# Optimization experiments

Hardware: AMD Instinct MI355X
Metric: run time of the kernel (lower is better)

The kernel has to match this reference:

```python
import jax, jax.numpy as jnp
import numpy as np

N_NODES = 50000
N_EDGES = 1_600_000
N_HEADS = 8
IN_DIM = 512
OUT_DIM = 64
LRELU_ALPHA = 0.2


def setup_inputs() -> dict:
    key = jax.random.key(0)
    k1, k2, k3, k4, k5 = jax.random.split(key, 5)
    x = jax.random.normal(k1, (N_NODES, IN_DIM), dtype=jnp.float32)
    # glorot-ish scale for weights
    W = jax.random.normal(k2, (N_HEADS, IN_DIM, OUT_DIM), dtype=jnp.float32) * (1.0 / np.sqrt(IN_DIM))
    att_w = jax.random.normal(k3, (N_HEADS, 2 * OUT_DIM), dtype=jnp.float32) * (1.0 / np.sqrt(2 * OUT_DIM))
    src = jax.random.randint(k4, (N_EDGES,), 0, N_NODES, dtype=jnp.int64 if jax.config.read('jax_enable_x64') else jnp.int32).astype(jnp.int32)
    dst = jax.random.randint(k5, (N_EDGES,), 0, N_NODES, dtype=jnp.int32)
    return {"x": x, "W": W, "att_w": att_w, "src": src, "dst": dst}


def reference(x, W, att_w, src, dst):
    # GAT forward (eval mode: dropout=0, bias off, heads concatenated).
    # attention score: leaky_relu([f_src || f_dst] @ a) == leaky_relu(a1.f_src + a2.f_dst)
    outs = []
    for h in range(N_HEADS):
        feat = x @ W[h]                               # [N, F]
        a1 = att_w[h, :OUT_DIM]                       # [F]
        a2 = att_w[h, OUT_DIM:]                       # [F]
        alpha_s = feat @ a1                           # [N]
        alpha_d = feat @ a2                           # [N]
        logit = jax.nn.leaky_relu(alpha_s[src] + alpha_d[dst], LRELU_ALPHA)  # [E]
        # sparse row-wise softmax over segments keyed by src (row index)
        m = jax.ops.segment_max(logit, src, num_segments=N_NODES)
        e = jnp.exp(logit - m[src])
        denom = jax.ops.segment_sum(e, src, num_segments=N_NODES)
        att = e / denom[src]                          # [E]
        # sparse-dense aggregation: out[row] = sum_edges att * feat[col]
        agg = jax.ops.segment_sum(att[:, None] * feat[dst], src, num_segments=N_NODES)  # [N, F]
        outs.append(jax.nn.relu(agg))                 # act per head (average_heads=False)
    return jnp.concatenate(outs, axis=1)              # [N, H*F]
```

## Files before the change

kernel.cpp:

```cpp
#include <hip/hip_runtime.h>
#include <math.h>

#define N_NODES   50000
#define N_EDGES   1600000
#define N_HEADS   8
#define IN_DIM    512
#define OUT_DIM   64
#define FEAT_DIM  512
#define LRELU_A   0.2f
#define M_TILES   391
#define M_PAD     (M_TILES*128)
#define SCAN_BLK  49

typedef __attribute__((ext_vector_type(8))) short bf16x8;
typedef __attribute__((ext_vector_type(4))) float f32x4;

__device__ inline unsigned short f2bf(float f) {
    unsigned int u = __float_as_uint(f);
    u = (u + 0x7FFFu + ((u >> 16) & 1u)) >> 16;
    return (unsigned short)u;
}
__device__ inline float bf2f(short s) {
    return __uint_as_float(((unsigned int)(unsigned short)s) << 16);
}

__global__ __launch_bounds__(256) void convert_x(const float* __restrict__ x,
                                                 unsigned short* __restrict__ xh) {
    int i = blockIdx.x * blockDim.x + threadIdx.x;
    if (i >= N_NODES * IN_DIM / 4) return;
    float4 v = ((const float4*)x)[i];
    ushort4 o;
    o.x = f2bf(v.x); o.y = f2bf(v.y); o.z = f2bf(v.z); o.w = f2bf(v.w);
    ((ushort4*)xh)[i] = o;
}

__global__ __launch_bounds__(256) void prep_b(const float* __restrict__ W,
                                              unsigned short* __restrict__ Bt) {
    int t = blockIdx.x * blockDim.x + threadIdx.x;
    if (t >= FEAT_DIM * IN_DIM) return;
    int n = t >> 9, k = t & 511;
    int h = n >> 6, o = n & 63;
    Bt[t] = f2bf(W[(size_t)h * IN_DIM * OUT_DIM + (size_t)k * OUT_DIM + o]);
}

__global__ __launch_bounds__(256) void gemm_mfma(const unsigned short* __restrict__ xh,
                                                 const unsigned short* __restrict__ Bt,
                                                 unsigned short* __restrict__ feat_h) {
    __shared__ __align__(16) unsigned short As[128 * 32];
    __shared__ __align__(16) unsigned short Bs[128 * 32];
    const int t    = threadIdx.x;
    const int wid  = t >> 6;
    const int lane = t & 63;
    const int m0   = blockIdx.x * 128;
    const int n0   = blockIdx.y * 128;
    const int wm   = (wid >> 1) * 64;
    const int wn   = (wid & 1) * 64;
    const int mr   = lane & 15;
    const int q    = lane >> 4;

    f32x4 acc[4][4];
    #pragma unroll
    for (int i = 0; i < 4; ++i)
        #pragma unroll
        for (int j = 0; j < 4; ++j) acc[i][j] = 0.0f;

    const char* xb = (const char*)xh;
    const char* bb = (const char*)Bt;
    const int o1 = t * 16;         const int row1 = o1 >> 6, kb1 = o1 & 63;
    const int o2 = t * 16 + 4096;  const int row2 = o2 >> 6, kb2 = o2 & 63;
    char* lA1 = ((char*)As) + wid * 1024;
    char* lA2 = ((char*)As) + 4096 + wid * 1024;
    char* lB1 = ((char*)Bs) + wid * 1024;
    char* lB2 = ((char*)Bs) + 4096 + wid * 1024;

    for (int k0 = 0; k0 < IN_DIM; k0 += 32) {
        const int kbyte = k0 * 2;
        __builtin_amdgcn_global_load_lds(
            (const __attribute__((address_space(1))) unsigned int*)(xb + (size_t)(m0 + row1) * (IN_DIM * 2) + kbyte + kb1),
            (__attribute__((address_space(3))) unsigned int*)lA1, 16, 0, 0);
        __builtin_amdgcn_global_load_lds(
            (const __attribute__((address_space(1))) unsigned int*)(xb + (size_t)(m0 + row2) * (IN_DIM * 2) + kbyte + kb2),
            (__attribute__((address_space(3))) unsigned int*)lA2, 16, 0, 0);
        __builtin_amdgcn_global_load_lds(
            (const __attribute__((address_space(1))) unsigned int*)(bb + (size_t)(n0 + row1) * (IN_DIM * 2) + kbyte + kb1),
            (__attribute__((address_space(3))) unsigned int*)lB1, 16, 0, 0);
        __builtin_amdgcn_global_load_lds(
            (const __attribute__((address_space(1))) unsigned int*)(bb + (size_t)(n0 + row2) * (IN_DIM * 2) + kbyte + kb2),
            (__attribute__((address_space(3))) unsigned int*)lB2, 16, 0, 0);
        __syncthreads();

        bf16x8 a[4], b[4];
        #pragma unroll
        for (int i = 0; i < 4; ++i)
            a[i] = *(const bf16x8*)&As[(wm + i * 16 + mr) * 32 + q * 8];
        #pragma unroll
        for (int j = 0; j < 4; ++j)
            b[j] = *(const bf16x8*)&Bs[(wn + j * 16 + mr) * 32 + q * 8];
        #pragma unroll
        for (int i = 0; i < 4; ++i)
            #pragma unroll
            for (int j = 0; j < 4; ++j)
                acc[i][j] = __builtin_amdgcn_mfma_f32_16x16x32_bf16(a[i], b[j], acc[i][j], 0, 0, 0);
        __syncthreads();
    }

    #pragma unroll
    for (int i = 0; i < 4; ++i) {
        #pragma unroll
        for (int j = 0; j < 4; ++j) {
            int col = n0 + wn + j * 16 + mr;
            #pragma unroll
            for (int r = 0; r < 4; ++r) {
                int row = m0 + wm + i * 16 + q * 4 + r;
                if (row < N_NODES)
                    feat_h[(size_t)row * FEAT_DIM + col] = f2bf(acc[i][j][r]);
            }
        }
    }
}

__global__ __launch_bounds__(256) void alpha_kernel(const unsigned short* __restrict__ feat_h,
                                                    const float* __restrict__ att_w,
                                                    float* __restrict__ alpha_s,
                                                    float* __restrict__ alpha_d) {
    int node = (blockIdx.x * blockDim.x + threadIdx.x) >> 6;
    int lane = threadIdx.x & 63;
    if (node >= N_NODES) return;
    int h   = lane >> 3;
    int sub = lane & 7;
    bf16x8 f = *(const bf16x8*)&feat_h[(size_t)node * FEAT_DIM + lane * 8];
    float s = 0.f, d = 0.f;
    #pragma unroll
    for (int i = 0; i < 8; ++i) {
        float fv = bf2f(f[i]);
        s += fv * att_w[h * 128 + sub * 8 + i];
        d += fv * att_w[h * 128 + 64 + sub * 8 + i];
    }
    #pragma unroll
    for (int off = 1; off < 8; off <<= 1) {
        s += __shfl_xor(s, off);
        d += __shfl_xor(d, off);
    }
    if (sub == 0) {
        alpha_s[node * N_HEADS + h] = s;
        alpha_d[node * N_HEADS + h] = d;
    }
}

__global__ __launch_bounds__(256) void count_kernel(const int* __restrict__ src,
                                                    int* __restrict__ cnt) {
    int e = (blockIdx.x * blockDim.x + threadIdx.x) * 4;
    if (e < N_EDGES) {
        int4 s = *(const int4*)&src[e];
        atomicAdd(&cnt[s.x], 1);
        atomicAdd(&cnt[s.y], 1);
        atomicAdd(&cnt[s.z], 1);
        atomicAdd(&cnt[s.w], 1);
    }
}

__global__ __launch_bounds__(1024) void scan_block_sums(const int* __restrict__ cnt,
                                                        int* __restrict__ partials) {
    __shared__ int wsum[16];
    const int t    = threadIdx.x;
    const int lane = t & 63;
    const int wid  = t >> 6;
    int i = blockIdx.x * 1024 + t;
    int v = (i < N_NODES) ? cnt[i] : 0;
    #pragma unroll
    for (int off = 32; off > 0; off >>= 1) v += __shfl_xor(v, off);
    if (lane == 0) wsum[wid] = v;
    __syncthreads();
    if (t < 16) {
        int u = wsum[t];
        #pragma unroll
        for (int off = 1; off < 16; off <<= 1) u += __shfl_xor(u, off);
        if (t == 0) partials[blockIdx.x] = u;
    }
}

__global__ __launch_bounds__(64) void scan_partials(const int* __restrict__ partials,
                                                    int* __restrict__ blkoff,
                                                    int* __restrict__ row_ptr) {
    int l = threadIdx.x;
    int v = (l < SCAN_BLK) ? partials[l] : 0;
    int incl = v;
    #pragma unroll
    for (int off = 1; off < 64; off <<= 1) {
        int u = __shfl_up(incl, off);
        if (l >= off) incl += u;
    }
    if (l < SCAN_BLK) blkoff[l] = incl - v;
    if (l == SCAN_BLK - 1) row_ptr[N_NODES] = incl;
}

__global__ __launch_bounds__(1024) void scan_apply(const int* __restrict__ cnt,
                                                   const int* __restrict__ blkoff,
                                                   int* __restrict__ row_ptr,
                                                   int* __restrict__ cursor) {
    __shared__ int wsum[16];
    const int t    = threadIdx.x;
    const int lane = t & 63;
    const int wid  = t >> 6;
    int i = blockIdx.x * 1024 + t;
    int v = (i < N_NODES) ? cnt[i] : 0;
    int incl = v;
    #pragma unroll
    for (int off = 1; off < 64; off <<= 1) {
        int u = __shfl_up(incl, off);
        if (lane >= off) incl += u;
    }
    if (lane == 63) wsum[wid] = incl;
    __syncthreads();
    if (t < 16) {
        int u = wsum[t];
        #pragma unroll
        for (int off = 1; off < 16; off <<= 1) {
            int w = __shfl_up(u, off);
            if (t >= off) u += w;
        }
        wsum[t] = u;
    }
    __syncthreads();
    int woff = (wid > 0) ? wsum[wid - 1] : 0;
    int excl = blkoff[blockIdx.x] + woff + incl - v;
    if (i < N_NODES) { row_ptr[i] = excl; cursor[i] = excl; }
}

__global__ __launch_bounds__(256) void scatter_kernel(const int* __restrict__ src,
                                                      const int* __restrict__ dst,
                                                      int* __restrict__ cursor,
                                                      int* __restrict__ csr_dst) {
    int e = (blockIdx.x * blockDim.x + threadIdx.x) * 4;
    if (e < N_EDGES) {
        int4 s = *(const int4*)&src[e];
        int4 d = *(const int4*)&dst[e];
        int p0 = atomicAdd(&cursor[s.x], 1); csr_dst[p0] = d.x;
        int p1 = atomicAdd(&cursor[s.y], 1); csr_dst[p1] = d.y;
        int p2 = atomicAdd(&cursor[s.z], 1); csr_dst[p2] = d.z;
        int p3 = atomicAdd(&cursor[s.w], 1); csr_dst[p3] = d.w;
    }
}

__global__ __launch_bounds__(256) void agg_kernel(const unsigned short* __restrict__ feat_h,
                                                  const float* __restrict__ alpha_s,
                                                  const float* __restrict__ alpha_d,
                                                  const int* __restrict__ row_ptr,
                                                  const int* __restrict__ csr_dst,
                                                  float* __restrict__ out) {
    __shared__ float red[2][64][9];
    const int wv   = __builtin_amdgcn_readfirstlane(threadIdx.x >> 6);
    const int lane = threadIdx.x & 63;
    const int node = blockIdx.x * 2 + (wv >> 1);
    const int half = wv & 1;
    const int h    = lane >> 3;

    const int start = row_ptr[node];
    const int end   = row_ptr[node + 1];
    const int deg   = end - start;
    const int lo    = start + ((deg * half) >> 1);
    const int hi    = start + ((deg * (half + 1)) >> 1);
    const int cnt2  = hi - lo;
    const float as  = alpha_s[node * N_HEADS + h];
    const int* cd   = csr_dst + lo;

    float sacc = 0.f;
    float acc[8] = {};

    int j = 0;
    for (; j + 8 <= cnt2; j += 8) {
        int d[8];
        #pragma unroll
        for (int k = 0; k < 8; ++k) d[k] = cd[j + k];
        float ad[8];
        #pragma unroll
        for (int k = 0; k < 8; ++k) ad[k] = alpha_d[(size_t)d[k] * N_HEADS + h];
        bf16x8 f[8];
        #pragma unroll
        for (int k = 0; k < 8; ++k)
            f[k] = *(const bf16x8*)&feat_h[(size_t)d[k] * FEAT_DIM + lane * 8];
        float e[8];
        #pragma unroll
        for (int k = 0; k < 8; ++k) {
            float z = as + ad[k];
            z = z > 0.f ? z : LRELU_A * z;
            e[k] = __expf(z);
        }
        sacc += ((e[0] + e[1]) + (e[2] + e[3])) + ((e[4] + e[5]) + (e[6] + e[7]));
        #pragma unroll
        for (int i = 0; i < 8; ++i) {
            float a = acc[i];
            #pragma unroll
            for (int k = 0; k < 8; ++k) a += e[k] * bf2f(f[k][i]);
            acc[i] = a;
        }
    }
    for (; j < cnt2; ++j) {
        int dd = cd[j];
        float ad0 = alpha_d[(size_t)dd * N_HEADS + h];
        bf16x8 f0 = *(const bf16x8*)&feat_h[(size_t)dd * FEAT_DIM + lane * 8];
        float z = as + ad0; z = z > 0.f ? z : LRELU_A * z;
        float e0 = __expf(z);
        sacc += e0;
        #pragma unroll
        for (int i = 0; i < 8; ++i) acc[i] += e0 * bf2f(f0[i]);
    }

    const int pr = wv >> 1;
    if (half == 1) {
        #pragma unroll
        for (int i = 0; i < 8; ++i) red[pr][lane][i] = acc[i];
        red[pr][lane][8] = sacc;
    }
    __syncthreads();
    if (half == 0) {
        #pragma unroll
        for (int i = 0; i < 8; ++i) acc[i] += red[pr][lane][i];
        sacc += red[pr][lane][8];
        const float inv = (deg > 0) ? 1.f / sacc : 0.f;
        f32x4 o0 = { fmaxf(acc[0] * inv, 0.f), fmaxf(acc[1] * inv, 0.f),
                     fmaxf(acc[2] * inv, 0.f), fmaxf(acc[3] * inv, 0.f) };
        f32x4 o1 = { fmaxf(acc[4] * inv, 0.f), fmaxf(acc[5] * inv, 0.f),
                     fmaxf(acc[6] * inv, 0.f), fmaxf(acc[7] * inv, 0.f) };
        f32x4* op = (f32x4*)(out + (size_t)node * FEAT_DIM + lane * 8);
        __builtin_nontemporal_store(o0, op);
        __builtin_nontemporal_store(o1, op + 1);
    }
}

extern "C" void kernel_launch(void* const* d_in, const int* in_sizes, int n_in,
                              void* d_out, int out_size, void* d_ws, size_t ws_size,
                              hipStream_t stream) {
    const float* x     = (const float*)d_in[0];
    const float* W     = (const float*)d_in[1];
    const float* att_w = (const float*)d_in[2];
    const int*   src   = (const int*)d_in[3];
    const int*   dst   = (const int*)d_in[4];
    float* out = (float*)d_out;

    char* ws = (char*)d_ws;
    size_t off = 0;
    auto alloc = [&](size_t bytes) {
        void* p = ws + off;
        off += (bytes + 255) & ~(size_t)255;
        return p;
    };
    unsigned short* feat_h = (unsigned short*)alloc((size_t)N_NODES * FEAT_DIM * sizeof(short));
    unsigned short* xh     = (unsigned short*)alloc((size_t)M_PAD * IN_DIM * sizeof(short));
    unsigned short* Bt     = (unsigned short*)alloc((size_t)FEAT_DIM * IN_DIM * sizeof(short));
    float* alpha_s = (float*)alloc((size_t)N_NODES * N_HEADS * sizeof(float));
    float* alpha_d = (float*)alloc((size_t)N_NODES * N_HEADS * sizeof(float));
    int*   cnt     = (int*)alloc((size_t)N_NODES * sizeof(int));
    int*   row_ptr = (int*)alloc((size_t)(N_NODES + 1) * sizeof(int));
    int*   cursor  = (int*)alloc((size_t)N_NODES * sizeof(int));
    int*   csr_dst = (int*)alloc((size_t)N_EDGES * sizeof(int));
    int*   partials = (int*)alloc((size_t)SCAN_BLK * sizeof(int));
    int*   blkoff   = (int*)alloc((size_t)SCAN_BLK * sizeof(int));

    (void)hipMemsetAsync(cnt, 0, (size_t)N_NODES * sizeof(int), stream);

    convert_x<<<(N_NODES * IN_DIM / 4 + 255) / 256, 256, 0, stream>>>(x, xh);
    prep_b<<<(FEAT_DIM * IN_DIM + 255) / 256, 256, 0, stream>>>(W, Bt);

    dim3 ggrid(M_TILES, FEAT_DIM / 128);
    gemm_mfma<<<ggrid, 256, 0, stream>>>(xh, Bt, feat_h);

    alpha_kernel<<<(N_NODES + 3) / 4, 256, 0, stream>>>(feat_h, att_w, alpha_s, alpha_d);

    count_kernel<<<(N_EDGES / 4 + 255) / 256, 256, 0, stream>>>(src, cnt);
    scan_block_sums<<<SCAN_BLK, 1024, 0, stream>>>(cnt, partials);
    scan_partials<<<1, 64, 0, stream>>>(partials, blkoff, row_ptr);
    scan_apply<<<SCAN_BLK, 1024, 0, stream>>>(cnt, blkoff, row_ptr, cursor);
    scatter_kernel<<<(N_EDGES / 4 + 255) / 256, 256, 0, stream>>>(src, dst, cursor, csr_dst);

    agg_kernel<<<N_NODES / 2, 256, 0, stream>>>(feat_h, alpha_s, alpha_d, row_ptr, csr_dst, out);
}
```

Measured before the change: 685.2 us.

## Bucket CSR edges by destination block and aggregate 8 nodes per wave in lockstep

Edges are now sorted by a composite key (src, dst>>11), giving 25 destination buckets per source node. The aggregation kernel has each wave handle 8 nodes and walk the buckets in order, so gathers of feat_h from concurrently running waves target a narrow range of rows. The goal is better L2 reuse of the gathered feature rows. In exchange the count/scan arrays grow 25x (1.25M keys), scan_partials loops serially, and each wave now handles 8 nodes at low unroll with large register arrays (acc[8][8]). That cuts occupancy and parallelism, since only about 1563 blocks are launched.

```diff
diff --git a/kernel.cpp b/kernel.cpp
--- a/kernel.cpp
+++ b/kernel.cpp
@@ -10,7 +10,11 @@
 #define LRELU_A   0.2f
 #define M_TILES   391
 #define M_PAD     (M_TILES*128)
-#define SCAN_BLK  49
+
+#define DBLK_SHIFT 11
+#define NBLK       25
+#define NKEYS      (N_NODES * NBLK)
+#define KSCAN_BLK  ((NKEYS + 1023) / 1024)
 
 typedef __attribute__((ext_vector_type(8))) short bf16x8;
 typedef __attribute__((ext_vector_type(4))) float f32x4;
@@ -148,14 +152,16 @@
 }
 
 __global__ __launch_bounds__(256) void count_kernel(const int* __restrict__ src,
+                                                    const int* __restrict__ dst,
                                                     int* __restrict__ cnt) {
     int e = (blockIdx.x * blockDim.x + threadIdx.x) * 4;
     if (e < N_EDGES) {
         int4 s = *(const int4*)&src[e];
-        atomicAdd(&cnt[s.x], 1);
-        atomicAdd(&cnt[s.y], 1);
-        atomicAdd(&cnt[s.z], 1);
-        atomicAdd(&cnt[s.w], 1);
+        int4 d = *(const int4*)&dst[e];
+        atomicAdd(&cnt[s.x * NBLK + (d.x >> DBLK_SHIFT)], 1);
+        atomicAdd(&cnt[s.y * NBLK + (d.y >> DBLK_SHIFT)], 1);
+        atomicAdd(&cnt[s.z * NBLK + (d.z >> DBLK_SHIFT)], 1);
+        atomicAdd(&cnt[s.w * NBLK + (d.w >> DBLK_SHIFT)], 1);
     }
 }
 
@@ -166,7 +172,7 @@
     const int lane = t & 63;
     const int wid  = t >> 6;
     int i = blockIdx.x * 1024 + t;
-    int v = (i < N_NODES) ? cnt[i] : 0;
+    int v = (i < NKEYS) ? cnt[i] : 0;
     #pragma unroll
     for (int off = 32; off > 0; off >>= 1) v += __shfl_xor(v, off);
     if (lane == 0) wsum[wid] = v;
@@ -179,31 +185,53 @@
     }
 }
 
-__global__ __launch_bounds__(64) void scan_partials(const int* __restrict__ partials,
-                                                    int* __restrict__ blkoff,
-                                                    int* __restrict__ row_ptr) {
-    int l = threadIdx.x;
-    int v = (l < SCAN_BLK) ? partials[l] : 0;
-    int incl = v;
-    #pragma unroll
-    for (int off = 1; off < 64; off <<= 1) {
-        int u = __shfl_up(incl, off);
-        if (l >= off) incl += u;
-    }
-    if (l < SCAN_BLK) blkoff[l] = incl - v;
-    if (l == SCAN_BLK - 1) row_ptr[N_NODES] = incl;
+__global__ __launch_bounds__(1024) void scan_partials(const int* __restrict__ partials,
+                                                      int* __restrict__ blkoff,
+                                                      int* __restrict__ keyptr) {
+    __shared__ int wsum[16];
+    const int t    = threadIdx.x;
+    const int lane = t & 63;
+    const int wid  = t >> 6;
+    int carry = 0;
+    for (int base = 0; base < KSCAN_BLK; base += 1024) {
+        int i = base + t;
+        int v = (i < KSCAN_BLK) ? partials[i] : 0;
+        int incl = v;
+        #pragma unroll
+        for (int off = 1; off < 64; off <<= 1) {
+            int u = __shfl_up(incl, off);
+            if (lane >= off) incl += u;
+        }
+        if (lane == 63) wsum[wid] = incl;
+        __syncthreads();
+        if (t < 16) {
+            int u = wsum[t];
+            #pragma unroll
+            for (int off = 1; off < 16; off <<= 1) {
+                int w = __shfl_up(u, off);
+                if (t >= off) u += w;
+            }
+            wsum[t] = u;
+        }
+        __syncthreads();
+        int woff = (wid > 0) ? wsum[wid - 1] : 0;
+        if (i < KSCAN_BLK) blkoff[i] = carry + woff + incl - v;
+        carry += wsum[15];
+        __syncthreads();
+    }
+    if (t == 0) keyptr[NKEYS] = carry;
 }
 
 __global__ __launch_bounds__(1024) void scan_apply(const int* __restrict__ cnt,
                                                    const int* __restrict__ blkoff,
-                                                   int* __restrict__ row_ptr,
+                                                   int* __restrict__ keyptr,
                                                    int* __restrict__ cursor) {
     __shared__ int wsum[16];
     const int t    = threadIdx.x;
     const int lane = t & 63;
     const int wid  = t >> 6;
     int i = blockIdx.x * 1024 + t;
-    int v = (i < N_NODES) ? cnt[i] : 0;
+    int v = (i < NKEYS) ? cnt[i] : 0;
     int incl = v;
     #pragma unroll
     for (int off = 1; off < 64; off <<= 1) {
@@ -224,7 +252,7 @@
     __syncthreads();
     int woff = (wid > 0) ? wsum[wid - 1] : 0;
     int excl = blkoff[blockIdx.x] + woff + incl - v;
-    if (i < N_NODES) { row_ptr[i] = excl; cursor[i] = excl; }
+    if (i < NKEYS) { keyptr[i] = excl; cursor[i] = excl; }
 }
 
 __global__ __launch_bounds__(256) void scatter_kernel(const int* __restrict__ src,
@@ -235,93 +263,80 @@
     if (e < N_EDGES) {
         int4 s = *(const int4*)&src[e];
         int4 d = *(const int4*)&dst[e];
-        int p0 = atomicAdd(&cursor[s.x], 1); csr_dst[p0] = d.x;
-        int p1 = atomicAdd(&cursor[s.y], 1); csr_dst[p1] = d.y;
-        int p2 = atomicAdd(&cursor[s.z], 1); csr_dst[p2] = d.z;
-        int p3 = atomicAdd(&cursor[s.w], 1); csr_dst[p3] = d.w;
+        int p0 = atomicAdd(&cursor[s.x * NBLK + (d.x >> DBLK_SHIFT)], 1); csr_dst[p0] = d.x;
+        int p1 = atomicAdd(&cursor[s.y * NBLK + (d.y >> DBLK_SHIFT)], 1); csr_dst[p1] = d.y;
+        int p2 = atomicAdd(&cursor[s.z * NBLK + (d.z >> DBLK_SHIFT)], 1); csr_dst[p2] = d.z;
+        int p3 = atomicAdd(&cursor[s.w * NBLK + (d.w >> DBLK_SHIFT)], 1); csr_dst[p3] = d.w;
     }
 }
 
 __global__ __launch_bounds__(256) void agg_kernel(const unsigned short* __restrict__ feat_h,
                                                   const float* __restrict__ alpha_s,
                                                   const float* __restrict__ alpha_d,
-                                                  const int* __restrict__ row_ptr,
+                                                  const int* __restrict__ keyptr,
                                                   const int* __restrict__ csr_dst,
                                                   float* __restrict__ out) {
-    __shared__ float red[2][64][9];
     const int wv   = __builtin_amdgcn_readfirstlane(threadIdx.x >> 6);
     const int lane = threadIdx.x & 63;
-    const int node = blockIdx.x * 2 + (wv >> 1);
-    const int half = wv & 1;
     const int h    = lane >> 3;
-
-    const int start = row_ptr[node];
-    const int end   = row_ptr[node + 1];
-    const int deg   = end - start;
-    const int lo    = start + ((deg * half) >> 1);
-    const int hi    = start + ((deg * (half + 1)) >> 1);
-    const int cnt2  = hi - lo;
-    const float as  = alpha_s[node * N_HEADS + h];
-    const int* cd   = csr_dst + lo;
-
-    float sacc = 0.f;
-    float acc[8] = {};
-
-    int j = 0;
-    for (; j + 8 <= cnt2; j += 8) {
-        int d[8];
-        #pragma unroll
-        for (int k = 0; k < 8; ++k) d[k] = cd[j + k];
-        float ad[8];
-        #pragma unroll
-        for (int k = 0; k < 8; ++k) ad[k] = alpha_d[(size_t)d[k] * N_HEADS + h];
-        bf16x8 f[8];
-        #pragma unroll
-        for (int k = 0; k < 8; ++k)
-            f[k] = *(const bf16x8*)&feat_h[(size_t)d[k] * FEAT_DIM + lane * 8];
-        float e[8];
-        #pragma unroll
-        for (int k = 0; k < 8; ++k) {
-            float z = as + ad[k];
-            z = z > 0.f ? z : LRELU_A * z;
-            e[k] = __expf(z);
-        }
-        sacc += ((e[0] + e[1]) + (e[2] + e[3])) + ((e[4] + e[5]) + (e[6] + e[7]));
-        #pragma unroll
-        for (int i = 0; i < 8; ++i) {
-            float a = acc[i];
-            #pragma unroll
-            for (int k = 0; k < 8; ++k) a += e[k] * bf2f(f[k][i]);
-            acc[i] = a;
-        }
-    }
-    for (; j < cnt2; ++j) {
-        int dd = cd[j];
-        float ad0 = alpha_d[(size_t)dd * N_HEADS + h];
-        bf16x8 f0 = *(const bf16x8*)&feat_h[(size_t)dd * FEAT_DIM + lane * 8];
-        float z = as + ad0; z = z > 0.f ? z : LRELU_A * z;
-        float e0 = __expf(z);
-        sacc += e0;
-        #pragma unroll
-        for (int i = 0; i < 8; ++i) acc[i] += e0 * bf2f(f0[i]);
-    }
-
-    const int pr = wv >> 1;
-    if (half == 1) {
-        #pragma unroll
-        for (int i = 0; i < 8; ++i) red[pr][lane][i] = acc[i];
-        red[pr][lane][8] = sacc;
-    }
-    __syncthreads();
-    if (half == 0) {
-        #pragma unroll
-        for (int i = 0; i < 8; ++i) acc[i] += red[pr][lane][i];
-        sacc += red[pr][lane][8];
-        const float inv = (deg > 0) ? 1.f / sacc : 0.f;
-        f32x4 o0 = { fmaxf(acc[0] * inv, 0.f), fmaxf(acc[1] * inv, 0.f),
-                     fmaxf(acc[2] * inv, 0.f), fmaxf(acc[3] * inv, 0.f) };
-        f32x4 o1 = { fmaxf(acc[4] * inv, 0.f), fmaxf(acc[5] * inv, 0.f),
-                     fmaxf(acc[6] * inv, 0.f), fmaxf(acc[7] * inv, 0.f) };
+    const int base = blockIdx.x * 32 + wv * 8;
+
+    float acc[8][8];
+    float sacc[8];
+    float as[8];
+    #pragma unroll
+    for (int n = 0; n < 8; ++n) {
+        sacc[n] = 0.f;
+        #pragma unroll
+        for (int i = 0; i < 8; ++i) acc[n][i] = 0.f;
+        int node = base + n;
+        as[n] = (node < N_NODES) ? alpha_s[node * N_HEADS + h] : 0.f;
+    }
+
+    for (int p = 0; p < NBLK; ++p) {
+        #pragma unroll
+        for (int n = 0; n < 8; ++n) {
+            const int node = base + n;
+            if (node >= N_NODES) continue;
+            const int b0 = keyptr[node * NBLK + p];
+            const int b1 = keyptr[node * NBLK + p + 1];
+            const float as_n = as[n];
+            int j = b0;
+            for (; j + 2 <= b1; j += 2) {
+                int d0 = csr_dst[j], d1 = csr_dst[j + 1];
+                float ad0 = alpha_d[d0 * N_HEADS + h];
+                float ad1 = alpha_d[d1 * N_HEADS + h];
+                bf16x8 f0 = *(const bf16x8*)&feat_h[(size_t)d0 * FEAT_DIM + lane * 8];
+                bf16x8 f1 = *(const bf16x8*)&feat_h[(size_t)d1 * FEAT_DIM + lane * 8];
+                float z0 = as_n + ad0; z0 = z0 > 0.f ? z0 : LRELU_A * z0; float e0 = __expf(z0);
+                float z1 = as_n + ad1; z1 = z1 > 0.f ? z1 : LRELU_A * z1; float e1 = __expf(z1);
+                sacc[n] += e0 + e1;
+                #pragma unroll
+                for (int i = 0; i < 8; ++i)
+                    acc[n][i] += e0 * bf2f(f0[i]) + e1 * bf2f(f1[i]);
+            }
+            if (j < b1) {
+                int d0 = csr_dst[j];
+                float ad0 = alpha_d[d0 * N_HEADS + h];
+                bf16x8 f0 = *(const bf16x8*)&feat_h[(size_t)d0 * FEAT_DIM + lane * 8];
+                float z0 = as_n + ad0; z0 = z0 > 0.f ? z0 : LRELU_A * z0; float e0 = __expf(z0);
+                sacc[n] += e0;
+                #pragma unroll
+                for (int i = 0; i < 8; ++i)
+                    acc[n][i] += e0 * bf2f(f0[i]);
+            }
+        }
+    }
+
+    #pragma unroll
+    for (int n = 0; n < 8; ++n) {
+        const int node = base + n;
+        if (node >= N_NODES) continue;
+        const float inv = (sacc[n] > 0.f) ? 1.f / sacc[n] : 0.f;
+        f32x4 o0 = { fmaxf(acc[n][0] * inv, 0.f), fmaxf(acc[n][1] * inv, 0.f),
+                     fmaxf(acc[n][2] * inv, 0.f), fmaxf(acc[n][3] * inv, 0.f) };
+        f32x4 o1 = { fmaxf(acc[n][4] * inv, 0.f), fmaxf(acc[n][5] * inv, 0.f),
+                     fmaxf(acc[n][6] * inv, 0.f), fmaxf(acc[n][7] * inv, 0.f) };
         f32x4* op = (f32x4*)(out + (size_t)node * FEAT_DIM + lane * 8);
         __builtin_nontemporal_store(o0, op);
         __builtin_nontemporal_store(o1, op + 1);
@@ -350,14 +365,14 @@
     unsigned short* Bt     = (unsigned short*)alloc((size_t)FEAT_DIM * IN_DIM * sizeof(short));
     float* alpha_s = (float*)alloc((size_t)N_NODES * N_HEADS * sizeof(float));
     float* alpha_d = (float*)alloc((size_t)N_NODES * N_HEADS * sizeof(float));
-    int*   cnt     = (int*)alloc((size_t)N_NODES * sizeof(int));
-    int*   row_ptr = (int*)alloc((size_t)(N_NODES + 1) * sizeof(int));
-    int*   cursor  = (int*)alloc((size_t)N_NODES * sizeof(int));
+    int*   cnt     = (int*)alloc((size_t)NKEYS * sizeof(int));
+    int*   keyptr  = (int*)alloc((size_t)(NKEYS + 1) * sizeof(int));
     int*   csr_dst = (int*)alloc((size_t)N_EDGES * sizeof(int));
-    int*   partials = (int*)alloc((size_t)SCAN_BLK * sizeof(int));
-    int*   blkoff   = (int*)alloc((size_t)SCAN_BLK * sizeof(int));
-
-    (void)hipMemsetAsync(cnt, 0, (size_t)N_NODES * sizeof(int), stream);
+    int*   partials = (int*)alloc((size_t)KSCAN_BLK * sizeof(int));
+    int*   blkoff   = (int*)alloc((size_t)KSCAN_BLK * sizeof(int));
+    int*   cursor   = cnt;
+
+    (void)hipMemsetAsync(cnt, 0, (size_t)NKEYS * sizeof(int), stream);
 
     convert_x<<<(N_NODES * IN_DIM / 4 + 255) / 256, 256, 0, stream>>>(x, xh);
     prep_b<<<(FEAT_DIM * IN_DIM + 255) / 256, 256, 0, stream>>>(W, Bt);
@@ -367,11 +382,11 @@
 
     alpha_kernel<<<(N_NODES + 3) / 4, 256, 0, stream>>>(feat_h, att_w, alpha_s, alpha_d);
 
-    count_kernel<<<(N_EDGES / 4 + 255) / 256, 256, 0, stream>>>(src, cnt);
-    scan_block_sums<<<SCAN_BLK, 1024, 0, stream>>>(cnt, partials);
-    scan_partials<<<1, 64, 0, stream>>>(partials, blkoff, row_ptr);
-    scan_apply<<<SCAN_BLK, 1024, 0, stream>>>(cnt, blkoff, row_ptr, cursor);
+    count_kernel<<<(N_EDGES / 4 + 255) / 256, 256, 0, stream>>>(src, dst, cnt);
+    scan_block_sums<<<KSCAN_BLK, 1024, 0, stream>>>(cnt, partials);
+    scan_partials<<<1, 1024, 0, stream>>>(partials, blkoff, keyptr);
+    scan_apply<<<KSCAN_BLK, 1024, 0, stream>>>(cnt, blkoff, keyptr, cursor);
     scatter_kernel<<<(N_EDGES / 4 + 255) / 256, 256, 0, stream>>>(src, dst, cursor, csr_dst);
 
-    agg_kernel<<<N_NODES / 2, 256, 0, stream>>>(feat_h, alpha_s, alpha_d, row_ptr, csr_dst, out);
-}
+    agg_kernel<<<(N_NODES + 31) / 32, 256, 0, stream>>>(feat_h, alpha_s, alpha_d, keyptr, csr_dst, out);
+}
```

Measured after the change: 752.6 us. 9.8% more time.
